# Kernel optimization log

Hardware: AMD Instinct MI355X
Metric: run time of the kernel (lower is better)

## Reference

```python
import jax, jax.numpy as jnp
import numpy as np

# Model dims (match init_kwargs)
N_P, NV, P, S = 60, 5, 20, 14   # particles, vertices, pf features, sv features
HID, DE, DO, NCLS, BATCH = 60, 20, 24, 2, 512

# Rr/Rs one-hot matrices encode edges (r, s) for r != s with r varying slowest.
# So gather-by-Rr == repeat each node N-1 times, gather-by-Rs == index by senders,
# and scatter-sum by Rr^T == reshape to [B, N, N-1, De] and sum axis 2.
_SENDERS = np.array([s for r in range(N_P) for s in range(N_P) if s != r])


def _lin_params(key, din, dout):
    kw, kb = jax.random.split(key)
    bound = 1.0 / np.sqrt(din)
    w = jax.random.uniform(kw, (din, dout), minval=-bound, maxval=bound, dtype=jnp.float32)
    b = jax.random.uniform(kb, (dout,), minval=-bound, maxval=bound, dtype=jnp.float32)
    return w, b


def setup_inputs() -> dict:
    key = jax.random.key(0)
    ks = jax.random.split(key, 12)
    inp = {
        'x': jax.random.normal(ks[0], (BATCH, P, N_P), dtype=jnp.float32),
        'y': jax.random.normal(ks[1], (BATCH, S, NV), dtype=jnp.float32),
    }
    specs = [('fr', [(2 * P, HID), (HID, HID), (HID, DE)]),
             ('pv', [(S + P, HID), (HID, HID), (HID, DE)]),
             ('fo', [(P + 2 * DE, HID), (HID, HID), (HID, DO)])]
    ki = 2
    for name, dims in specs:
        for j, (di, do) in enumerate(dims, 1):
            w, b = _lin_params(ks[ki], di, do)
            ki += 1
            inp[f'{name}_w{j}'] = w
            inp[f'{name}_b{j}'] = b
    w, b = _lin_params(ks[11], DO, NCLS)
    inp['fc_w'] = w
    inp['fc_b'] = b
    return inp


def _mlp3(h, w1, b1, w2, b2, w3, b3):
    h = jax.nn.relu(h @ w1 + b1)
    h = jax.nn.relu(h @ w2 + b2)
    return jax.nn.relu(h @ w3 + b3)


def reference(x, y, fr_w1, fr_b1, fr_w2, fr_b2, fr_w3, fr_b3,
              pv_w1, pv_b1, pv_w2, pv_b2, pv_w3, pv_b3,
              fo_w1, fo_b1, fo_w2, fo_b2, fo_w3, fo_b3, fc_w, fc_b):
    xt = jnp.swapaxes(x, -1, -2)  # [B, N, P]
    yt = jnp.swapaxes(y, -1, -2)  # [B, Nv, S]
    B = xt.shape[0]

    # particle-particle edge conv (gather via index, scatter-sum via reshape)
    Orr = jnp.repeat(xt, N_P - 1, axis=1)          # [B, Nr, P], receiver features
    Ors = xt[:, _SENDERS]                          # [B, Nr, P], sender features
    E = _mlp3(jnp.concatenate([Orr, Ors], axis=-1),
              fr_w1, fr_b1, fr_w2, fr_b2, fr_w3, fr_b3)  # [B, Nr, De]
    Ebar_pp = E.reshape(B, N_P, N_P - 1, DE).sum(axis=2)  # [B, N, De]

    # particle-vertex edge conv (Rk repeats particles, Rv tiles vertices)
    Ork = jnp.repeat(xt, NV, axis=1)               # [B, Nt, P]
    Orv = jnp.tile(yt, (1, N_P, 1))                # [B, Nt, S]
    E2 = _mlp3(jnp.concatenate([Ork, Orv], axis=-1),
               pv_w1, pv_b1, pv_w2, pv_b2, pv_w3, pv_b3)  # [B, Nt, De]
    Ebar_pv = E2.reshape(B, N_P, NV, DE).sum(axis=2)      # [B, N, De]

    C = jnp.concatenate([xt, Ebar_pp, Ebar_pv], axis=-1)  # [B, N, P + 2*De]
    O = _mlp3(C, fo_w1, fo_b1, fo_w2, fo_b2, fo_w3, fo_b3)  # [B, N, Do]
    return O.sum(axis=-2) @ fc_w + fc_b  # [B, num_classes]
```

## Files before the change

kernel.cpp:

```cpp
#include <hip/hip_runtime.h>

#define BATCH 512
#define NPART 60
#define PFEAT 20
#define SFEAT 14
#define NVTX  5
#define HID   60
#define DE    20
#define DO    24
#define NCLS  2
#define SR    68

typedef _Float16 half8  __attribute__((ext_vector_type(8)));
typedef _Float16 half4v __attribute__((ext_vector_type(4)));
typedef __fp16   fp16x2 __attribute__((ext_vector_type(2)));
typedef float    f32x4  __attribute__((ext_vector_type(4)));

__device__ __forceinline__ half4v pkcvt4(f32x4 a) {
    fp16x2 lo = __builtin_amdgcn_cvt_pkrtz(a[0], a[1]);
    fp16x2 hi = __builtin_amdgcn_cvt_pkrtz(a[2], a[3]);
    half4v r;
    r[0] = (_Float16)lo[0]; r[1] = (_Float16)lo[1];
    r[2] = (_Float16)hi[0]; r[3] = (_Float16)hi[1];
    return r;
}
__device__ __forceinline__ half4v relu4(half4v a) {
#pragma unroll
    for (int j = 0; j < 4; ++j)
        a[j] = (a[j] > (_Float16)0.f) ? a[j] : (_Float16)0.f;
    return a;
}
__device__ __forceinline__ f32x4 bias4(const float* b, int col4, int lim) {
    f32x4 z = {0.f, 0.f, 0.f, 0.f};
    return (col4 < lim) ? *(const f32x4*)(b + col4) : z;
}

__global__ __launch_bounds__(256) void prep_kernel(
    const float* __restrict__ x,
    const float* __restrict__ fr_w1, const float* __restrict__ pv_w1,
    const float* __restrict__ fr_w2, const float* __restrict__ fr_w3,
    const float* __restrict__ pv_w2, const float* __restrict__ pv_w3,
    const float* __restrict__ fo_w1, const float* __restrict__ fo_w2,
    const float* __restrict__ fo_w3,
    _Float16* __restrict__ frW2p, _Float16* __restrict__ frW3p16,
    _Float16* __restrict__ pvW2p, _Float16* __restrict__ pvW3p16,
    _Float16* __restrict__ foW1p, _Float16* __restrict__ foW2p16,
    _Float16* __restrict__ foW3p16,
    _Float16* __restrict__ frW1Ap, _Float16* __restrict__ frW1Bp,
    _Float16* __restrict__ pvW1Ap, _Float16* __restrict__ xp)
{
    if (blockIdx.x < 16) {
        int idx = blockIdx.x*256 + threadIdx.x;
        {
            int j  = idx & 7;
            int L  = (idx >> 3) & 63;
            int kk = (idx >> 9) & 1;
            int u  = idx >> 10;
            int k  = kk*32 + (L >> 4)*8 + j;
            int n  = u*16 + (L & 15);
            bool ok = (k < HID && n < HID);
            frW2p[idx] = (_Float16)(ok ? fr_w2[k*HID + n] : 0.f);
            pvW2p[idx] = (_Float16)(ok ? pv_w2[k*HID + n] : 0.f);
            foW1p[idx] = (_Float16)(ok ? fo_w1[k*HID + n] : 0.f);
        }
        {
            int j  = idx & 3;
            int L  = (idx >> 2) & 63;
            int kt = (idx >> 8) & 3;
            int u  = idx >> 10;
            int k  = kt*16 + (L >> 4)*4 + j;
            int n  = u*16 + (L & 15);
            foW2p16[idx] = (_Float16)((k < HID && n < HID) ? fo_w2[k*HID + n] : 0.f);
        }
        if (idx < 2048) {
            {
                int j  = idx & 3;
                int L  = (idx >> 2) & 63;
                int kt = (idx >> 8) & 3;
                int u  = idx >> 10;
                int k  = kt*16 + (L >> 4)*4 + j;
                int n  = u*16 + (L & 15);
                frW3p16[idx] = (_Float16)((k < HID && n < DE) ? fr_w3[k*DE + n] : 0.f);
                pvW3p16[idx] = (_Float16)((k < HID && n < DE) ? pv_w3[k*DE + n] : 0.f);
                foW3p16[idx] = (_Float16)((k < HID && n < DO) ? fo_w3[k*DO + n] : 0.f);
            }
            {
                int j = idx & 7;
                int L = (idx >> 3) & 63;
                int u = idx >> 9;
                int k = (L >> 4)*8 + j;
                int n = u*16 + (L & 15);
                bool ok = (k < PFEAT && n < HID);
                frW1Ap[idx] = (_Float16)(ok ? fr_w1[k*HID + n] : 0.f);
                frW1Bp[idx] = (_Float16)(ok ? fr_w1[(PFEAT + k)*HID + n] : 0.f);
                pvW1Ap[idx] = (_Float16)(ok ? pv_w1[k*HID + n] : 0.f);
            }
        }
    } else {
        int idx = (blockIdx.x - 16)*256 + threadIdx.x;
        if (idx < BATCH*NPART*4) {
            int p = idx % NPART;
            int t = idx / NPART;
            int q = t & 3;
            int b = t >> 2;
            half8 v;
#pragma unroll
            for (int j = 0; j < 8; ++j) {
                int k = q*8 + j;
                v[j] = (_Float16)((k < PFEAT) ? x[((size_t)b*PFEAT + k)*NPART + p] : 0.f);
            }
            *(half8*)(xp + ((size_t)b*NPART + p)*32 + q*8) = v;
        }
    }
}

__global__ __launch_bounds__(512) void fused_kernel(
    const float* __restrict__ y,
    const float* __restrict__ fr_b1,
    const float* __restrict__ fr_b2, const float* __restrict__ fr_b3,
    const float* __restrict__ pv_w1, const float* __restrict__ pv_b1,
    const float* __restrict__ pv_b2, const float* __restrict__ pv_b3,
    const float* __restrict__ fo_b1, const float* __restrict__ fo_b2,
    const float* __restrict__ fo_b3,
    const float* __restrict__ fcw, const float* __restrict__ fcb,
    const half8*  __restrict__ frw2p, const half4v* __restrict__ frw3p16,
    const half8*  __restrict__ pvw2p, const half4v* __restrict__ pvw3p16,
    const half8*  __restrict__ fow1p, const half4v* __restrict__ fow2p16,
    const half4v* __restrict__ fow3p16,
    const half8*  __restrict__ frw1ap, const half8* __restrict__ frw1bp,
    const half8*  __restrict__ pvw1ap, const _Float16* __restrict__ xp,
    float* __restrict__ out)
{
    __shared__ __align__(16) _Float16 sFrA[NPART*SR];
    __shared__ __align__(16) _Float16 sFrB[NPART*SR];
    __shared__ __align__(16) _Float16 sPvA[NPART*SR];
    __shared__ __align__(16) _Float16 sPvV[NVTX*64];
    __shared__ __align__(16) _Float16 sEpp[NPART*DE];
    __shared__ __align__(16) _Float16 sEpvP[NVTX*NPART*DE];
    __shared__ __align__(16) float    sDsum[4][DO];
    _Float16* sCin = sFrA;

    int bb   = blockIdx.x;
    int wv   = threadIdx.x >> 6;
    int lane = threadIdx.x & 63;
    int ml   = lane & 15;
    int q    = lane >> 4;

    {
        int tile = wv & 3;
        int row  = 16*tile + ml;
        int rr   = (row < NPART) ? row : 0;
        half8 bX = *(const half8*)(xp + ((size_t)bb*NPART + rr)*32 + q*8);
#pragma unroll
        for (int task = 0; task < 2; ++task) {
            const half8* Wt; const float* bset; _Float16* Ot;
            if (wv < 4) {
                if (task == 0) { Wt = frw1ap; bset = fr_b1;  Ot = sFrA; }
                else           { Wt = pvw1ap; bset = nullptr; Ot = sPvA; }
            } else {
                if (task == 1) break;
                Wt = frw1bp; bset = nullptr; Ot = sFrB;
            }
#pragma unroll
            for (int u = 0; u < 4; ++u) {
                half8 w8 = Wt[u*64 + lane];
                f32x4 acc = bset ? bias4(bset, u*16 + 4*q, HID - 3)
                                 : (f32x4){0.f, 0.f, 0.f, 0.f};
                acc = __builtin_amdgcn_mfma_f32_16x16x32_f16(w8, bX, acc, 0, 0, 0);
                if (row < NPART)
                    *(half4v*)(Ot + row*SR + u*16 + 4*q) = pkcvt4(acc);
            }
        }
        for (int idx = threadIdx.x; idx < NVTX*64; idx += 512) {
            int v = idx >> 6;
            int h = idx & 63;
            float a = 0.f;
            if (h < HID) {
                a = pv_b1[h];
#pragma unroll
                for (int f = 0; f < SFEAT; ++f)
                    a += y[((size_t)bb*SFEAT + f)*NVTX + v] * pv_w1[(PFEAT + f)*HID + h];
            }
            sPvV[idx] = (_Float16)a;
        }
    }
    __syncthreads();

    for (int r = wv; r < NPART; r += 8) {
        float s[2][4];
#pragma unroll
        for (int v = 0; v < 2; ++v)
#pragma unroll
            for (int i = 0; i < 4; ++i) s[v][i] = 0.f;

#pragma unroll
        for (int th = 0; th < 2; ++th) {
            half8 bA[2][2];
#pragma unroll
            for (int tl = 0; tl < 2; ++tl) {
                int edge = 16*(2*th + tl) + ml;
                int sr = (edge < NPART-1) ? (edge + (edge >= r)) : 0;
#pragma unroll
                for (int kk = 0; kk < 2; ++kk) {
                    half8 u8 = *(const half8*)(sFrA + r*SR + kk*32 + q*8);
                    half8 v8 = *(const half8*)(sFrB + sr*SR + kk*32 + q*8);
                    half8 s8 = u8 + v8;
#pragma unroll
                    for (int j = 0; j < 8; ++j) {
                        _Float16 vj = s8[j];
                        s8[j] = (vj > (_Float16)0.f) ? vj : (_Float16)0.f;
                    }
                    bA[tl][kk] = s8;
                }
            }
            f32x4 acc3[2][2];
#pragma unroll
            for (int v = 0; v < 2; ++v) {
                f32x4 bi = bias4(fr_b3, v*16 + 4*q, DE - 3);
#pragma unroll
                for (int tl = 0; tl < 2; ++tl) acc3[v][tl] = bi;
            }
#pragma unroll
            for (int u = 0; u < 4; ++u) {
                half8 w0 = frw2p[(u*2 + 0)*64 + lane];
                half8 w1 = frw2p[(u*2 + 1)*64 + lane];
                f32x4 bi2 = bias4(fr_b2, u*16 + 4*q, HID - 3);
                half4v a3u[2];
#pragma unroll
                for (int tl = 0; tl < 2; ++tl) {
                    f32x4 a = bi2;
                    a = __builtin_amdgcn_mfma_f32_16x16x32_f16(w0, bA[tl][0], a, 0, 0, 0);
                    a = __builtin_amdgcn_mfma_f32_16x16x32_f16(w1, bA[tl][1], a, 0, 0, 0);
                    a3u[tl] = relu4(pkcvt4(a));
                }
                half4v w3a = frw3p16[(0*4 + u)*64 + lane];
                half4v w3b = frw3p16[(1*4 + u)*64 + lane];
#pragma unroll
                for (int tl = 0; tl < 2; ++tl) {
                    acc3[0][tl] = __builtin_amdgcn_mfma_f32_16x16x16f16(w3a, a3u[tl], acc3[0][tl], 0, 0, 0);
                    acc3[1][tl] = __builtin_amdgcn_mfma_f32_16x16x16f16(w3b, a3u[tl], acc3[1][tl], 0, 0, 0);
                }
            }
#pragma unroll
            for (int v = 0; v < 2; ++v)
#pragma unroll
                for (int tl = 0; tl < 2; ++tl) {
                    int edge = 16*(2*th + tl) + ml;
                    bool ok = edge < NPART-1;
#pragma unroll
                    for (int i = 0; i < 4; ++i)
                        s[v][i] += ok ? fmaxf(acc3[v][tl][i], 0.f) : 0.f;
                }
        }
#pragma unroll
        for (int v = 0; v < 2; ++v) {
#pragma unroll
            for (int i = 0; i < 4; ++i) {
                s[v][i] += __shfl_xor(s[v][i], 1);
                s[v][i] += __shfl_xor(s[v][i], 2);
                s[v][i] += __shfl_xor(s[v][i], 4);
                s[v][i] += __shfl_xor(s[v][i], 8);
            }
            int col4 = v*16 + 4*q;
            if (ml == 0 && col4 < DE) {
                f32x4 o = {s[v][0], s[v][1], s[v][2], s[v][3]};
                *(half4v*)(sEpp + r*DE + col4) = pkcvt4(o);
            }
        }
    }

    if (wv < NVTX) {
        int gv = wv;
#pragma unroll
        for (int th = 0; th < 2; ++th) {
            half8 bA[2][2];
#pragma unroll
            for (int tl = 0; tl < 2; ++tl) {
                int p = 16*(2*th + tl) + ml;
                int sr = (p < NPART) ? p : 0;
#pragma unroll
                for (int kk = 0; kk < 2; ++kk) {
                    half8 u8 = *(const half8*)(sPvV + gv*64 + kk*32 + q*8);
                    half8 v8 = *(const half8*)(sPvA + sr*SR + kk*32 + q*8);
                    half8 s8 = u8 + v8;
#pragma unroll
                    for (int j = 0; j < 8; ++j) {
                        _Float16 vj = s8[j];
                        s8[j] = (vj > (_Float16)0.f) ? vj : (_Float16)0.f;
                    }
                    bA[tl][kk] = s8;
                }
            }
            f32x4 acc3[2][2];
#pragma unroll
            for (int v = 0; v < 2; ++v) {
                f32x4 bi = bias4(pv_b3, v*16 + 4*q, DE - 3);
#pragma unroll
                for (int tl = 0; tl < 2; ++tl) acc3[v][tl] = bi;
            }
#pragma unroll
            for (int u = 0; u < 4; ++u) {
                half8 w0 = pvw2p[(u*2 + 0)*64 + lane];
                half8 w1 = pvw2p[(u*2 + 1)*64 + lane];
                f32x4 bi2 = bias4(pv_b2, u*16 + 4*q, HID - 3);
                half4v a3u[2];
#pragma unroll
                for (int tl = 0; tl < 2; ++tl) {
                    f32x4 a = bi2;
                    a = __builtin_amdgcn_mfma_f32_16x16x32_f16(w0, bA[tl][0], a, 0, 0, 0);
                    a = __builtin_amdgcn_mfma_f32_16x16x32_f16(w1, bA[tl][1], a, 0, 0, 0);
                    a3u[tl] = relu4(pkcvt4(a));
                }
                half4v w3a = pvw3p16[(0*4 + u)*64 + lane];
                half4v w3b = pvw3p16[(1*4 + u)*64 + lane];
#pragma unroll
                for (int tl = 0; tl < 2; ++tl) {
                    acc3[0][tl] = __builtin_amdgcn_mfma_f32_16x16x16f16(w3a, a3u[tl], acc3[0][tl], 0, 0, 0);
                    acc3[1][tl] = __builtin_amdgcn_mfma_f32_16x16x16f16(w3b, a3u[tl], acc3[1][tl], 0, 0, 0);
                }
            }
#pragma unroll
            for (int v = 0; v < 2; ++v) {
                int col4 = v*16 + 4*q;
#pragma unroll
                for (int tl = 0; tl < 2; ++tl) {
                    int p = 16*(2*th + tl) + ml;
                    if (p < NPART && col4 < DE) {
                        half4v hv = relu4(pkcvt4(acc3[v][tl]));
                        *(half4v*)(sEpvP + (gv*NPART + p)*DE + col4) = hv;
                    }
                }
            }
        }
    }
    __syncthreads();

    for (int idx = threadIdx.x; idx < NPART*64; idx += 512) {
        int p = idx >> 6;
        int k = idx & 63;
        _Float16 v;
        if (k < PFEAT) {
            v = xp[((size_t)bb*NPART + p)*32 + k];
        } else if (k < PFEAT + DE) {
            v = sEpp[p*DE + (k - PFEAT)];
        } else if (k < PFEAT + 2*DE) {
            int c = k - PFEAT - DE;
            float s = 0.f;
#pragma unroll
            for (int g5 = 0; g5 < NVTX; ++g5)
                s += (float)sEpvP[(g5*NPART + p)*DE + c];
            v = (_Float16)s;
        } else {
            v = (_Float16)0.f;
        }
        sCin[p*SR + k] = v;
    }
    __syncthreads();

    if (wv < 4) {
        int p = 16*wv + ml;
        int sp = (p < NPART) ? p : 0;
        half8 bC[2];
#pragma unroll
        for (int kk = 0; kk < 2; ++kk)
            bC[kk] = *(const half8*)(sCin + sp*SR + kk*32 + q*8);

        f32x4 acc1[4];
#pragma unroll
        for (int u = 0; u < 4; ++u) {
            acc1[u] = bias4(fo_b1, u*16 + 4*q, HID - 3);
            acc1[u] = __builtin_amdgcn_mfma_f32_16x16x32_f16(fow1p[(u*2 + 0)*64 + lane], bC[0], acc1[u], 0, 0, 0);
            acc1[u] = __builtin_amdgcn_mfma_f32_16x16x32_f16(fow1p[(u*2 + 1)*64 + lane], bC[1], acc1[u], 0, 0, 0);
        }
        half4v a2[4];
#pragma unroll
        for (int u = 0; u < 4; ++u) a2[u] = relu4(pkcvt4(acc1[u]));

        f32x4 acc2[4];
#pragma unroll
        for (int u = 0; u < 4; ++u) {
            acc2[u] = bias4(fo_b2, u*16 + 4*q, HID - 3);
#pragma unroll
            for (int kt = 0; kt < 4; ++kt)
                acc2[u] = __builtin_amdgcn_mfma_f32_16x16x16f16(fow2p16[(u*4 + kt)*64 + lane], a2[kt], acc2[u], 0, 0, 0);
        }
        half4v a3[4];
#pragma unroll
        for (int u = 0; u < 4; ++u) a3[u] = relu4(pkcvt4(acc2[u]));

        f32x4 acc3[2];
#pragma unroll
        for (int v = 0; v < 2; ++v) {
            acc3[v] = bias4(fo_b3, v*16 + 4*q, DO - 3);
#pragma unroll
            for (int u = 0; u < 4; ++u)
                acc3[v] = __builtin_amdgcn_mfma_f32_16x16x16f16(fow3p16[(v*4 + u)*64 + lane], a3[u], acc3[v], 0, 0, 0);
        }
#pragma unroll
        for (int v = 0; v < 2; ++v) {
            float s[4];
            bool ok = p < NPART;
#pragma unroll
            for (int i = 0; i < 4; ++i)
                s[i] = ok ? fmaxf(acc3[v][i], 0.f) : 0.f;
#pragma unroll
            for (int i = 0; i < 4; ++i) {
                s[i] += __shfl_xor(s[i], 1);
                s[i] += __shfl_xor(s[i], 2);
                s[i] += __shfl_xor(s[i], 4);
                s[i] += __shfl_xor(s[i], 8);
            }
            int col4 = v*16 + 4*q;
            if (ml == 0 && col4 < DO) {
                f32x4 o = {s[0], s[1], s[2], s[3]};
                *(f32x4*)(sDsum[wv] + col4) = o;
            }
        }
    }
    __syncthreads();

    if (wv == 0) {
        float tot = 0.f;
        if (lane < DO) {
#pragma unroll
            for (int w4 = 0; w4 < 4; ++w4) tot += sDsum[w4][lane];
        }
        float p0 = (lane < DO) ? tot * fcw[lane*NCLS + 0] : 0.f;
        float p1 = (lane < DO) ? tot * fcw[lane*NCLS + 1] : 0.f;
#pragma unroll
        for (int d = 1; d <= 16; d <<= 1) {
            p0 += __shfl_xor(p0, d);
            p1 += __shfl_xor(p1, d);
        }
        if (lane == 0) {
            out[bb*NCLS + 0] = p0 + fcb[0];
            out[bb*NCLS + 1] = p1 + fcb[1];
        }
    }
}

extern "C" void kernel_launch(void* const* d_in, const int* in_sizes, int n_in,
                              void* d_out, int out_size, void* d_ws, size_t ws_size,
                              hipStream_t stream)
{
    const float* x     = (const float*)d_in[0];
    const float* y     = (const float*)d_in[1];
    const float* fr_w1 = (const float*)d_in[2];
    const float* fr_b1 = (const float*)d_in[3];
    const float* fr_w2 = (const float*)d_in[4];
    const float* fr_b2 = (const float*)d_in[5];
    const float* fr_w3 = (const float*)d_in[6];
    const float* fr_b3 = (const float*)d_in[7];
    const float* pv_w1 = (const float*)d_in[8];
    const float* pv_b1 = (const float*)d_in[9];
    const float* pv_w2 = (const float*)d_in[10];
    const float* pv_b2 = (const float*)d_in[11];
    const float* pv_w3 = (const float*)d_in[12];
    const float* pv_b3 = (const float*)d_in[13];
    const float* fo_w1 = (const float*)d_in[14];
    const float* fo_b1 = (const float*)d_in[15];
    const float* fo_w2 = (const float*)d_in[16];
    const float* fo_b2 = (const float*)d_in[17];
    const float* fo_w3 = (const float*)d_in[18];
    const float* fo_b3 = (const float*)d_in[19];
    const float* fc_w  = (const float*)d_in[20];
    const float* fc_b  = (const float*)d_in[21];
    float* out = (float*)d_out;

    char* wsb = (char*)d_ws;
    size_t off = 0;
    auto alloc = [&](size_t bytes) { char* p = wsb + off; off += (bytes + 255) & ~(size_t)255; return p; };

    _Float16* frW2p   = (_Float16*)alloc(4096*2);
    _Float16* frW3p16 = (_Float16*)alloc(2048*2);
    _Float16* pvW2p   = (_Float16*)alloc(4096*2);
    _Float16* pvW3p16 = (_Float16*)alloc(2048*2);
    _Float16* foW1p   = (_Float16*)alloc(4096*2);
    _Float16* foW2p16 = (_Float16*)alloc(4096*2);
    _Float16* foW3p16 = (_Float16*)alloc(2048*2);
    _Float16* frW1Ap  = (_Float16*)alloc(2048*2);
    _Float16* frW1Bp  = (_Float16*)alloc(2048*2);
    _Float16* pvW1Ap  = (_Float16*)alloc(2048*2);
    _Float16* xp      = (_Float16*)alloc((size_t)BATCH*NPART*32*2);

    int xblocks = (BATCH*NPART*4 + 255)/256;
    prep_kernel<<<16 + xblocks, 256, 0, stream>>>(
        x, fr_w1, pv_w1,
        fr_w2, fr_w3, pv_w2, pv_w3, fo_w1, fo_w2, fo_w3,
        frW2p, frW3p16, pvW2p, pvW3p16, foW1p, foW2p16, foW3p16,
        frW1Ap, frW1Bp, pvW1Ap, xp);

    fused_kernel<<<BATCH, 512, 0, stream>>>(
        y, fr_b1, fr_b2, fr_b3,
        pv_w1, pv_b1, pv_b2, pv_b3,
        fo_b1, fo_b2, fo_b3, fc_w, fc_b,
        (const half8*)frW2p, (const half4v*)frW3p16,
        (const half8*)pvW2p, (const half4v*)pvW3p16,
        (const half8*)foW1p, (const half4v*)foW2p16, (const half4v*)foW3p16,
        (const half8*)frW1Ap, (const half8*)frW1Bp,
        (const half8*)pvW1Ap, xp,
        out);
}
```

Baseline: 152.0 us.

## Hoist MLP weights into registers, stage biases in LDS, relayout packed x

Edge-MLP layer-2/3 weight fragments are loaded once per wave into registers, pinned with empty asm, and reused across all receiver iterations. Previously they were reloaded from global memory for every receiver row. Biases are zero-padded into a shared-memory table so the guarded global bias4 reads disappear. The receiver-row features are hoisted out of the edge loop, the masked accumulate becomes an fma with a 0/1 factor, and the packed x buffer is relaid out as [b][q][p][8] for coalesced writes. Keeping the weights resident raises register pressure, which may reduce occupancy.

```diff
diff --git a/kernel.cpp b/kernel.cpp
--- a/kernel.cpp
+++ b/kernel.cpp
@@ -109,7 +109,7 @@
                 int k = q*8 + j;
                 v[j] = (_Float16)((k < PFEAT) ? x[((size_t)b*PFEAT + k)*NPART + p] : 0.f);
             }
-            *(half8*)(xp + ((size_t)b*NPART + p)*32 + q*8) = v;
+            *(half8*)(xp + (size_t)idx*8) = v;
         }
     }
 }
@@ -138,6 +138,7 @@
     __shared__ __align__(16) _Float16 sEpp[NPART*DE];
     __shared__ __align__(16) _Float16 sEpvP[NVTX*NPART*DE];
     __shared__ __align__(16) float    sDsum[4][DO];
+    __shared__ __align__(16) float    sBias[7*64];
     _Float16* sCin = sFrA;
 
     int bb   = blockIdx.x;
@@ -147,10 +148,23 @@
     int q    = lane >> 4;
 
     {
+        if (threadIdx.x < 448) {
+            int arr = wv, i = lane;
+            float bv = 0.f;
+            if      (arr == 0) { if (i < HID) bv = fr_b2[i]; }
+            else if (arr == 1) { if (i < DE)  bv = fr_b3[i]; }
+            else if (arr == 2) { if (i < HID) bv = pv_b2[i]; }
+            else if (arr == 3) { if (i < DE)  bv = pv_b3[i]; }
+            else if (arr == 4) { if (i < HID) bv = fo_b1[i]; }
+            else if (arr == 5) { if (i < HID) bv = fo_b2[i]; }
+            else               { if (i < DO)  bv = fo_b3[i]; }
+            sBias[threadIdx.x] = bv;
+        }
+
         int tile = wv & 3;
         int row  = 16*tile + ml;
         int rr   = (row < NPART) ? row : 0;
-        half8 bX = *(const half8*)(xp + ((size_t)bb*NPART + rr)*32 + q*8);
+        half8 bX = *(const half8*)(xp + (((size_t)bb*4 + q)*NPART + rr)*8);
 #pragma unroll
         for (int task = 0; task < 2; ++task) {
             const half8* Wt; const float* bset; _Float16* Ot;
@@ -186,25 +200,130 @@
     }
     __syncthreads();
 
-    for (int r = wv; r < NPART; r += 8) {
-        float s[2][4];
-#pragma unroll
-        for (int v = 0; v < 2; ++v)
-#pragma unroll
-            for (int i = 0; i < 4; ++i) s[v][i] = 0.f;
-
+    {
+        half8  w2r[8];
+        half4v w3r[8];
+#pragma unroll
+        for (int t = 0; t < 8; ++t) w2r[t] = frw2p[t*64 + lane];
+#pragma unroll
+        for (int t = 0; t < 8; ++t) w3r[t] = frw3p16[t*64 + lane];
+#pragma unroll
+        for (int t = 0; t < 8; ++t) {
+            asm volatile("" : "+v"(w2r[t]));
+            asm volatile("" : "+v"(w3r[t]));
+        }
+
+        for (int r = wv; r < NPART; r += 8) {
+            half8 u8k0 = *(const half8*)(sFrA + r*SR + q*8);
+            half8 u8k1 = *(const half8*)(sFrA + r*SR + 32 + q*8);
+            float s[2][4];
+#pragma unroll
+            for (int v = 0; v < 2; ++v)
+#pragma unroll
+                for (int i = 0; i < 4; ++i) s[v][i] = 0.f;
+
+#pragma unroll
+            for (int th = 0; th < 2; ++th) {
+                half8 bA[2][2];
+                float okf[2];
+#pragma unroll
+                for (int tl = 0; tl < 2; ++tl) {
+                    int edge = 16*(2*th + tl) + ml;
+                    bool eok = (edge < NPART-1);
+                    okf[tl] = eok ? 1.f : 0.f;
+                    int sr = eok ? (edge + (edge >= r)) : 0;
+#pragma unroll
+                    for (int kk = 0; kk < 2; ++kk) {
+                        half8 v8 = *(const half8*)(sFrB + sr*SR + kk*32 + q*8);
+                        half8 s8 = (kk ? u8k1 : u8k0) + v8;
+#pragma unroll
+                        for (int j = 0; j < 8; ++j) {
+                            _Float16 vj = s8[j];
+                            s8[j] = (vj > (_Float16)0.f) ? vj : (_Float16)0.f;
+                        }
+                        bA[tl][kk] = s8;
+                    }
+                }
+                f32x4 acc3[2][2];
+#pragma unroll
+                for (int v = 0; v < 2; ++v) {
+                    f32x4 bi = *(const f32x4*)(sBias + 1*64 + v*16 + 4*q);
+#pragma unroll
+                    for (int tl = 0; tl < 2; ++tl) acc3[v][tl] = bi;
+                }
+#pragma unroll
+                for (int u = 0; u < 4; ++u) {
+                    half8 w0 = w2r[u*2 + 0];
+                    half8 w1 = w2r[u*2 + 1];
+                    f32x4 bi2 = *(const f32x4*)(sBias + 0*64 + u*16 + 4*q);
+                    half4v a3u[2];
+#pragma unroll
+                    for (int tl = 0; tl < 2; ++tl) {
+                        f32x4 a = bi2;
+                        a = __builtin_amdgcn_mfma_f32_16x16x32_f16(w0, bA[tl][0], a, 0, 0, 0);
+                        a = __builtin_amdgcn_mfma_f32_16x16x32_f16(w1, bA[tl][1], a, 0, 0, 0);
+                        a3u[tl] = relu4(pkcvt4(a));
+                    }
+                    half4v w3a = w3r[0*4 + u];
+                    half4v w3b = w3r[1*4 + u];
+#pragma unroll
+                    for (int tl = 0; tl < 2; ++tl) {
+                        acc3[0][tl] = __builtin_amdgcn_mfma_f32_16x16x16f16(w3a, a3u[tl], acc3[0][tl], 0, 0, 0);
+                        acc3[1][tl] = __builtin_amdgcn_mfma_f32_16x16x16f16(w3b, a3u[tl], acc3[1][tl], 0, 0, 0);
+                    }
+                }
+#pragma unroll
+                for (int v = 0; v < 2; ++v)
+#pragma unroll
+                    for (int tl = 0; tl < 2; ++tl)
+#pragma unroll
+                        for (int i = 0; i < 4; ++i)
+                            s[v][i] = fmaf(fmaxf(acc3[v][tl][i], 0.f), okf[tl], s[v][i]);
+            }
+#pragma unroll
+            for (int v = 0; v < 2; ++v) {
+#pragma unroll
+                for (int i = 0; i < 4; ++i) {
+                    s[v][i] += __shfl_xor(s[v][i], 1);
+                    s[v][i] += __shfl_xor(s[v][i], 2);
+                    s[v][i] += __shfl_xor(s[v][i], 4);
+                    s[v][i] += __shfl_xor(s[v][i], 8);
+                }
+                int col4 = v*16 + 4*q;
+                if (ml == 0 && col4 < DE) {
+                    f32x4 o = {s[v][0], s[v][1], s[v][2], s[v][3]};
+                    *(half4v*)(sEpp + r*DE + col4) = pkcvt4(o);
+                }
+            }
+        }
+    }
+
+    if (wv < NVTX) {
+        int gv = wv;
+        half8  w2r[8];
+        half4v w3r[8];
+#pragma unroll
+        for (int t = 0; t < 8; ++t) w2r[t] = pvw2p[t*64 + lane];
+#pragma unroll
+        for (int t = 0; t < 8; ++t) w3r[t] = pvw3p16[t*64 + lane];
+#pragma unroll
+        for (int t = 0; t < 8; ++t) {
+            asm volatile("" : "+v"(w2r[t]));
+            asm volatile("" : "+v"(w3r[t]));
+        }
+        half8 u8k0 = *(const half8*)(sPvV + gv*64 + q*8);
+        half8 u8k1 = *(const half8*)(sPvV + gv*64 + 32 + q*8);
 #pragma unroll
         for (int th = 0; th < 2; ++th) {
             half8 bA[2][2];
 #pragma unroll
             for (int tl = 0; tl < 2; ++tl) {
-                int edge = 16*(2*th + tl) + ml;
-                int sr = (edge < NPART-1) ? (edge + (edge >= r)) : 0;
+                int p = 16*(2*th + tl) + ml;
+                int sr = (p < NPART) ? p : 0;
 #pragma unroll
                 for (int kk = 0; kk < 2; ++kk) {
-                    half8 u8 = *(const half8*)(sFrA + r*SR + kk*32 + q*8);
-                    half8 v8 = *(const half8*)(sFrB + sr*SR + kk*32 + q*8);
-                    half8 s8 = u8 + v8;
+                    half8 v8 = *(const half8*)(sPvA + sr*SR + kk*32 + q*8);
+                    half8 s8 = (kk ? u8k1 : u8k0) + v8;
 #pragma unroll
                     for (int j = 0; j < 8; ++j) {
                         _Float16 vj = s8[j];
@@ -216,15 +335,15 @@
             f32x4 acc3[2][2];
 #pragma unroll
             for (int v = 0; v < 2; ++v) {
-                f32x4 bi = bias4(fr_b3, v*16 + 4*q, DE - 3);
+                f32x4 bi = *(const f32x4*)(sBias + 3*64 + v*16 + 4*q);
 #pragma unroll
                 for (int tl = 0; tl < 2; ++tl) acc3[v][tl] = bi;
             }
 #pragma unroll
             for (int u = 0; u < 4; ++u) {
-                half8 w0 = frw2p[(u*2 + 0)*64 + lane];
-                half8 w1 = frw2p[(u*2 + 1)*64 + lane];
-                f32x4 bi2 = bias4(fr_b2, u*16 + 4*q, HID - 3);
+                half8 w0 = w2r[u*2 + 0];
+                half8 w1 = w2r[u*2 + 1];
+                f32x4 bi2 = *(const f32x4*)(sBias + 2*64 + u*16 + 4*q);
                 half4v a3u[2];
 #pragma unroll
                 for (int tl = 0; tl < 2; ++tl) {
@@ -233,86 +352,8 @@
                     a = __builtin_amdgcn_mfma_f32_16x16x32_f16(w1, bA[tl][1], a, 0, 0, 0);
                     a3u[tl] = relu4(pkcvt4(a));
                 }
-                half4v w3a = frw3p16[(0*4 + u)*64 + lane];
-                half4v w3b = frw3p16[(1*4 + u)*64 + lane];
-#pragma unroll
-                for (int tl = 0; tl < 2; ++tl) {
-                    acc3[0][tl] = __builtin_amdgcn_mfma_f32_16x16x16f16(w3a, a3u[tl], acc3[0][tl], 0, 0, 0);
-                    acc3[1][tl] = __builtin_amdgcn_mfma_f32_16x16x16f16(w3b, a3u[tl], acc3[1][tl], 0, 0, 0);
-                }
-            }
-#pragma unroll
-            for (int v = 0; v < 2; ++v)
-#pragma unroll
-                for (int tl = 0; tl < 2; ++tl) {
-                    int edge = 16*(2*th + tl) + ml;
-                    bool ok = edge < NPART-1;
-#pragma unroll
-                    for (int i = 0; i < 4; ++i)
-                        s[v][i] += ok ? fmaxf(acc3[v][tl][i], 0.f) : 0.f;
-                }
-        }
-#pragma unroll
-        for (int v = 0; v < 2; ++v) {
-#pragma unroll
-            for (int i = 0; i < 4; ++i) {
-                s[v][i] += __shfl_xor(s[v][i], 1);
-                s[v][i] += __shfl_xor(s[v][i], 2);
-                s[v][i] += __shfl_xor(s[v][i], 4);
-                s[v][i] += __shfl_xor(s[v][i], 8);
-            }
-            int col4 = v*16 + 4*q;
-            if (ml == 0 && col4 < DE) {
-                f32x4 o = {s[v][0], s[v][1], s[v][2], s[v][3]};
-                *(half4v*)(sEpp + r*DE + col4) = pkcvt4(o);
-            }
-        }
-    }
-
-    if (wv < NVTX) {
-        int gv = wv;
-#pragma unroll
-        for (int th = 0; th < 2; ++th) {
-            half8 bA[2][2];
-#pragma unroll
-            for (int tl = 0; tl < 2; ++tl) {
-                int p = 16*(2*th + tl) + ml;
-                int sr = (p < NPART) ? p : 0;
-#pragma unroll
-                for (int kk = 0; kk < 2; ++kk) {
-                    half8 u8 = *(const half8*)(sPvV + gv*64 + kk*32 + q*8);
-                    half8 v8 = *(const half8*)(sPvA + sr*SR + kk*32 + q*8);
-                    half8 s8 = u8 + v8;
-#pragma unroll
-                    for (int j = 0; j < 8; ++j) {
-                        _Float16 vj = s8[j];
-                        s8[j] = (vj > (_Float16)0.f) ? vj : (_Float16)0.f;
-                    }
-                    bA[tl][kk] = s8;
-                }
-            }
-            f32x4 acc3[2][2];
-#pragma unroll
-            for (int v = 0; v < 2; ++v) {
-                f32x4 bi = bias4(pv_b3, v*16 + 4*q, DE - 3);
-#pragma unroll
-                for (int tl = 0; tl < 2; ++tl) acc3[v][tl] = bi;
-            }
-#pragma unroll
-            for (int u = 0; u < 4; ++u) {
-                half8 w0 = pvw2p[(u*2 + 0)*64 + lane];
-                half8 w1 = pvw2p[(u*2 + 1)*64 + lane];
-                f32x4 bi2 = bias4(pv_b2, u*16 + 4*q, HID - 3);
-                half4v a3u[2];
-#pragma unroll
-                for (int tl = 0; tl < 2; ++tl) {
-                    f32x4 a = bi2;
-                    a = __builtin_amdgcn_mfma_f32_16x16x32_f16(w0, bA[tl][0], a, 0, 0, 0);
-                    a = __builtin_amdgcn_mfma_f32_16x16x32_f16(w1, bA[tl][1], a, 0, 0, 0);
-                    a3u[tl] = relu4(pkcvt4(a));
-                }
-                half4v w3a = pvw3p16[(0*4 + u)*64 + lane];
-                half4v w3b = pvw3p16[(1*4 + u)*64 + lane];
+                half4v w3a = w3r[0*4 + u];
+                half4v w3b = w3r[1*4 + u];
 #pragma unroll
                 for (int tl = 0; tl < 2; ++tl) {
                     acc3[0][tl] = __builtin_amdgcn_mfma_f32_16x16x16f16(w3a, a3u[tl], acc3[0][tl], 0, 0, 0);
@@ -340,7 +381,7 @@
         int k = idx & 63;
         _Float16 v;
         if (k < PFEAT) {
-            v = xp[((size_t)bb*NPART + p)*32 + k];
+            v = xp[(((size_t)bb*4 + (k >> 3))*NPART + p)*8 + (k & 7)];
         } else if (k < PFEAT + DE) {
             v = sEpp[p*DE + (k - PFEAT)];
         } else if (k < PFEAT + 2*DE) {
@@ -368,7 +409,7 @@
         f32x4 acc1[4];
 #pragma unroll
         for (int u = 0; u < 4; ++u) {
-            acc1[u] = bias4(fo_b1, u*16 + 4*q, HID - 3);
+            acc1[u] = *(const f32x4*)(sBias + 4*64 + u*16 + 4*q);
             acc1[u] = __builtin_amdgcn_mfma_f32_16x16x32_f16(fow1p[(u*2 + 0)*64 + lane], bC[0], acc1[u], 0, 0, 0);
             acc1[u] = __builtin_amdgcn_mfma_f32_16x16x32_f16(fow1p[(u*2 + 1)*64 + lane], bC[1], acc1[u], 0, 0, 0);
         }
@@ -379,7 +420,7 @@
         f32x4 acc2[4];
 #pragma unroll
         for (int u = 0; u < 4; ++u) {
-            acc2[u] = bias4(fo_b2, u*16 + 4*q, HID - 3);
+            acc2[u] = *(const f32x4*)(sBias + 5*64 + u*16 + 4*q);
 #pragma unroll
             for (int kt = 0; kt < 4; ++kt)
                 acc2[u] = __builtin_amdgcn_mfma_f32_16x16x16f16(fow2p16[(u*4 + kt)*64 + lane], a2[kt], acc2[u], 0, 0, 0);
@@ -391,7 +432,7 @@
         f32x4 acc3[2];
 #pragma unroll
         for (int v = 0; v < 2; ++v) {
-            acc3[v] = bias4(fo_b3, v*16 + 4*q, DO - 3);
+            acc3[v] = *(const f32x4*)(sBias + 6*64 + v*16 + 4*q);
 #pragma unroll
             for (int u = 0; u < 4; ++u)
                 acc3[v] = __builtin_amdgcn_mfma_f32_16x16x16f16(fow3p16[(v*4 + u)*64 + lane], a3[u], acc3[v], 0, 0, 0);
```

Result: no change. 150.6 us (-0.9%).
